# Optimization experiments

Measured on AMD Instinct MI355X. Metric: run time of the kernel, lower is better.

## Reference

```python
import jax, jax.numpy as jnp
import numpy as np

N_HEAD = 16
HEAD_DIM = 64  # n_embd // n_head = 1024 // 16

def setup_inputs() -> dict:
    key = jax.random.key(0)
    k1, k2, k3 = jax.random.split(key, 3)
    B, T, C = 4, 2048, 1024
    x = jax.random.normal(k1, (B, T, C), dtype=jnp.float32)
    w_qkv = jax.random.normal(k2, (3 * C, C), dtype=jnp.float32) * (C ** -0.5)
    w_proj = jax.random.normal(k3, (C, C), dtype=jnp.float32) * (C ** -0.5)
    b_proj = jnp.zeros((C,), dtype=jnp.float32)
    return {"x": x, "w_qkv": w_qkv, "w_proj": w_proj, "b_proj": b_proj}

def reference(x, w_qkv, w_proj, b_proj):
    B, T, C = x.shape
    H, hd = N_HEAD, HEAD_DIM
    # fused QKV projection (no bias), torch Linear: x @ W^T
    qkv = jnp.einsum('btc,dc->btd', x, w_qkv)           # [B,T,3C]
    # module-specific reshape: per-head groups of 3*hd, then chunk into q,k,v
    qkv = qkv.reshape(B, T, H, 3 * hd)
    q, k, v = jnp.split(qkv, 3, axis=-1)                # each [B,T,H,hd]
    q = q.transpose(0, 2, 1, 3)                         # [B,H,T,hd]
    k = k.transpose(0, 2, 1, 3)
    v = v.transpose(0, 2, 1, 3)
    att = jnp.einsum('bhqd,bhkd->bhqk', q, k) * (hd ** -0.5)
    causal = jnp.tril(jnp.ones((T, T), dtype=bool))
    att = jnp.where(causal, att, -jnp.inf)
    att = jax.nn.softmax(att, axis=-1)
    out = jnp.einsum('bhqk,bhkd->bhqd', att, v)         # [B,H,T,hd]
    out = out.transpose(0, 2, 1, 3).reshape(B, T, C)
    out = jnp.einsum('btc,dc->btd', out, w_proj) + b_proj
    return out
```

## Files before the change

### kernel.cpp

```cpp
#include <hip/hip_runtime.h>
#include <hip/hip_bf16.h>

typedef __attribute__((ext_vector_type(8))) short bf16x8;
typedef __attribute__((ext_vector_type(4))) float f32x4;
typedef __attribute__((ext_vector_type(16))) float f32x16;
typedef __attribute__((ext_vector_type(4))) int i32x4;
typedef unsigned short u16;

__device__ __forceinline__ u16 f2bf(float f) {
    __hip_bfloat16 h = __float2bfloat16(f);
    return __builtin_bit_cast(u16, h);
}
__device__ __forceinline__ bf16x8 load8(const u16* p) {
    return *reinterpret_cast<const bf16x8*>(p);
}
__device__ __forceinline__ void gl2lds16(const u16* g, u16* l) {
    __builtin_amdgcn_global_load_lds(
        (const __attribute__((address_space(1))) void*)g,
        (__attribute__((address_space(3))) void*)l, 16, 0, 0);
}
__device__ __forceinline__ unsigned int cvtpk(float lo, float hi) {
    unsigned int r;
    asm("v_cvt_pk_bf16_f32 %0, %1, %2" : "=v"(r) : "v"(lo), "v"(hi));
    return r;
}

#define QSCALE 0.1803368801111244f

__global__ __launch_bounds__(256) void cast_f32_bf16(
    const float* __restrict__ src, u16* __restrict__ dst, int n4)
{
    int i = blockIdx.x * blockDim.x + threadIdx.x;
    if (i < n4) {
        float4 f = reinterpret_cast<const float4*>(src)[i];
        ushort4 o;
        o.x = f2bf(f.x); o.y = f2bf(f.y); o.z = f2bf(f.z); o.w = f2bf(f.w);
        reinterpret_cast<ushort4*>(dst)[i] = o;
    }
}

#define GEMM128_BODY(EPILOGUE)                                                 \
    __shared__ __align__(16) u16 As[128 * 32];                                 \
    __shared__ __align__(16) u16 Bs[128 * 32];                                 \
    const int t = threadIdx.x;                                                 \
    const int lane = t & 63;                                                   \
    const int wave = t >> 6;                                                   \
    const int quad = lane >> 4;                                                \
    const int lid  = lane & 15;                                                \
    const int wrow = wave & 1;                                                 \
    const int wcol = wave >> 1;                                                \
    const int mtile = blockIdx.x * 128;                                        \
    const int ntile = blockIdx.y * 128;                                        \
    const int srow = t >> 2;                                                   \
    const int scol = (t & 3) * 8;                                              \
    const u16* ga0 = Aptr + (size_t)(mtile + srow) * 1024 + scol;              \
    const u16* ga1 = Aptr + (size_t)(mtile + 64 + srow) * 1024 + scol;         \
    const u16* gb0 = Bptr + (size_t)(ntile + srow) * 1024 + scol;              \
    const u16* gb1 = Bptr + (size_t)(ntile + 64 + srow) * 1024 + scol;         \
    u16* la0 = As + t * 8;                                                     \
    u16* la1 = As + (256 + t) * 8;                                             \
    u16* lb0 = Bs + t * 8;                                                     \
    u16* lb1 = Bs + (256 + t) * 8;                                             \
    f32x4 acc[4][4] = {};                                                      \
    const int aro = wrow * 64 * 32 + quad * 8;                                 \
    const int bro = wcol * 64 * 32 + quad * 8;                                 \
    for (int k0 = 0; k0 < 1024; k0 += 32) {                                    \
        __syncthreads();                                                       \
        gl2lds16(ga0 + k0, la0);                                               \
        gl2lds16(ga1 + k0, la1);                                               \
        gl2lds16(gb0 + k0, lb0);                                               \
        gl2lds16(gb1 + k0, lb1);                                               \
        __syncthreads();                                                       \
        bf16x8 a[4], b[4];                                                     \
        _Pragma("unroll")                                                      \
        for (int i = 0; i < 4; ++i) {                                          \
            a[i] = load8(As + aro + (i * 16 + lid) * 32);                      \
            b[i] = load8(Bs + bro + (i * 16 + lid) * 32);                      \
        }                                                                      \
        _Pragma("unroll")                                                      \
        for (int mi = 0; mi < 4; ++mi)                                         \
            _Pragma("unroll")                                                  \
            for (int ni = 0; ni < 4; ++ni)                                     \
                acc[mi][ni] = __builtin_amdgcn_mfma_f32_16x16x32_bf16(         \
                    a[mi], b[ni], acc[mi][ni], 0, 0, 0);                       \
    }                                                                          \
    EPILOGUE

__global__ __launch_bounds__(256) void qkv_gemm128(
    const u16* __restrict__ Aptr, const u16* __restrict__ Bptr,
    u16* __restrict__ Q, u16* __restrict__ K, u16* __restrict__ Vt)
{
    GEMM128_BODY(
    _Pragma("unroll")
    for (int mi = 0; mi < 4; ++mi)
        _Pragma("unroll")
        for (int ni = 0; ni < 4; ++ni)
            _Pragma("unroll")
            for (int r = 0; r < 4; ++r) {
                int m = mtile + wrow * 64 + mi * 16 + quad * 4 + r;
                int n = ntile + wcol * 64 + ni * 16 + lid;
                int h = n / 192;
                int rr = n - h * 192;
                int sel = rr >> 6;
                int d = rr & 63;
                float v = acc[mi][ni][r];
                if (sel == 2)
                    Vt[((size_t)h * 64 + d) * 8192 + m] = f2bf(v);
                else if (sel == 0)
                    Q[((size_t)h * 8192 + m) * 64 + d] = f2bf(v * QSCALE);
                else
                    K[((size_t)h * 8192 + m) * 64 + d] = f2bf(v);
            }
    )
}

__global__ __launch_bounds__(256) void proj_gemm128(
    const u16* __restrict__ Aptr, const u16* __restrict__ Bptr,
    const float* __restrict__ bias, float* __restrict__ out)
{
    GEMM128_BODY(
    _Pragma("unroll")
    for (int mi = 0; mi < 4; ++mi)
        _Pragma("unroll")
        for (int ni = 0; ni < 4; ++ni)
            _Pragma("unroll")
            for (int r = 0; r < 4; ++r) {
                int m = mtile + wrow * 64 + mi * 16 + quad * 4 + r;
                int n = ntile + wcol * 64 + ni * 16 + lid;
                out[(size_t)m * 1024 + n] = acc[mi][ni][r] + bias[n];
            }
    )
}

__global__ __launch_bounds__(256, 4) void attn(
    const u16* __restrict__ Q, const u16* __restrict__ K,
    const u16* __restrict__ Vtg, u16* __restrict__ O)
{
    const int qtile = 15 - (blockIdx.x >> 6);
    const int bh = blockIdx.x & 63;
    const int b = bh >> 4, h = bh & 15;
    const int tid = threadIdx.x;
    const int lane = tid & 63;
    const int wave = tid >> 6;
    const int c31 = lane & 31;
    const int ht  = lane >> 5;

    const size_t hb = ((size_t)h * 8192 + (size_t)b * 2048) * 64;
    const u16* Qp = Q + hb;
    const u16* Kp = K + hb;
    const u16* Vp = Vtg + (size_t)h * 64 * 8192 + (size_t)b * 2048;

    __shared__ __align__(16) u16 Vt[2][64 * 64];

    const int vd = tid >> 3, vslot = tid & 7;
    const int vchunk = vslot ^ (vd & 7);
    const u16* vg0 = Vp + (size_t)vd * 8192 + vchunk * 8;
    const u16* vg1 = vg0 + (size_t)32 * 8192;

    const int qb = qtile * 128;
    const int qw = qb + wave * 32;
    const int q  = qw + c31;

    bf16x8 qf[4];
#pragma unroll
    for (int dm = 0; dm < 4; ++dm)
        qf[dm] = load8(Qp + (size_t)q * 64 + dm * 16 + ht * 8);

    f32x16 od0 = {}, od1 = {};
    float lsum = 0.f;

    const int nkt   = 2 * qtile + 2;
    const int nkt_w = 2 * qtile + ((wave < 2) ? 1 : 2);

    gl2lds16(vg0, Vt[0] + tid * 8);
    gl2lds16(vg1, Vt[0] + 2048 + tid * 8);

#define SOFTMAX_KB(ST, KBOFF, PF0, PF1)                                        \
    {                                                                          \
        float pv[16];                                                          \
        _Pragma("unroll")                                                      \
        for (int r = 0; r < 16; ++r) {                                         \
            const int kg = k0 + (KBOFF) + (r & 3) + 8 * (r >> 2) + 4 * ht;     \
            float sv = ST[r];                                                  \
            if (needmask && kg > q) sv = -1e30f;                               \
            const float p = exp2f(sv);                                         \
            pv[r] = p;                                                         \
            lsum += p;                                                         \
        }                                                                      \
        _Pragma("unroll")                                                      \
        for (int a = 0; a < 2; ++a) {                                          \
            unsigned int u  = cvtpk(pv[8 * a + 0], pv[8 * a + 1]);             \
            unsigned int u2 = cvtpk(pv[8 * a + 2], pv[8 * a + 3]);             \
            unsigned int v  = cvtpk(pv[8 * a + 4], pv[8 * a + 5]);             \
            unsigned int v2 = cvtpk(pv[8 * a + 6], pv[8 * a + 7]);             \
            int r1 = __shfl_xor((int)(ht ? u : v), 32, 64);                    \
            int r2 = __shfl_xor((int)(ht ? u2 : v2), 32, 64);                  \
            i32x4 w;                                                           \
            w.x = ht ? r1 : (int)u;                                            \
            w.y = ht ? r2 : (int)u2;                                           \
            w.z = ht ? (int)v : r1;                                            \
            w.w = ht ? (int)v2 : r2;                                           \
            ((a) ? (PF1) : (PF0)) = __builtin_bit_cast(bf16x8, w);             \
        }                                                                      \
    }

    for (int kt = 0; kt < nkt; ++kt) {
        const int k0 = kt * 64;
        u16* vbuf = Vt[kt & 1];
        const bool active = kt < nkt_w;
        bf16x8 pf[4];

        if (active) {
            const bool needmask = (k0 + 63 > qw);
            bf16x8 kfA[4], kfB[4];
#pragma unroll
            for (int dm = 0; dm < 4; ++dm)
                kfA[dm] = load8(Kp + (size_t)(k0 + c31) * 64 + dm * 16 + ht * 8);
#pragma unroll
            for (int dm = 0; dm < 4; ++dm)
                kfB[dm] = load8(Kp + (size_t)(k0 + 32 + c31) * 64 + dm * 16 + ht * 8);

            f32x16 stA = {}, stB = {};
            __builtin_amdgcn_s_setprio(1);
#pragma unroll
            for (int dm = 0; dm < 4; ++dm)
                stA = __builtin_amdgcn_mfma_f32_32x32x16_bf16(kfA[dm], qf[dm], stA, 0, 0, 0);
#pragma unroll
            for (int dm = 0; dm < 4; ++dm)
                stB = __builtin_amdgcn_mfma_f32_32x32x16_bf16(kfB[dm], qf[dm], stB, 0, 0, 0);
            __builtin_amdgcn_s_setprio(0);

            SOFTMAX_KB(stA, 0,  pf[0], pf[1]);
            SOFTMAX_KB(stB, 32, pf[2], pf[3]);
        }

        __syncthreads();

        if (kt + 1 < nkt) {
            const int kn = k0 + 64;
            u16* vnext = Vt[(kt + 1) & 1];
            gl2lds16(vg0 + kn, vnext + tid * 8);
            gl2lds16(vg1 + kn, vnext + 2048 + tid * 8);
        }

        if (active) {
            __builtin_amdgcn_s_setprio(1);
#pragma unroll
            for (int km = 0; km < 4; ++km) {
                const int sl = ((km * 2 + ht) ^ (c31 & 7)) * 8;
                bf16x8 v0 = load8(vbuf + c31 * 64 + sl);
                bf16x8 v1 = load8(vbuf + (32 + c31) * 64 + sl);
                od0 = __builtin_amdgcn_mfma_f32_32x32x16_bf16(v0, pf[km], od0, 0, 0, 0);
                od1 = __builtin_amdgcn_mfma_f32_32x32x16_bf16(v1, pf[km], od1, 0, 0, 0);
            }
            __builtin_amdgcn_s_setprio(0);
        }
    }

    const float tot = lsum +
        __builtin_bit_cast(float, __shfl_xor(__builtin_bit_cast(int, lsum), 32, 64));
    const float inv = 1.0f / tot;

    const size_t orow = (size_t)(b * 2048 + q) * 1024 + h * 64;
#pragma unroll
    for (int tp = 0; tp < 8; ++tp) {
        const int r = 2 * tp;
        const int d = (r & 3) + 8 * (r >> 2) + 4 * ht;
        unsigned int w0 = (unsigned int)f2bf(od0[r] * inv) |
                          ((unsigned int)f2bf(od0[r + 1] * inv) << 16);
        unsigned int w1 = (unsigned int)f2bf(od1[r] * inv) |
                          ((unsigned int)f2bf(od1[r + 1] * inv) << 16);
        *reinterpret_cast<unsigned int*>(const_cast<u16*>(O) + orow + d) = w0;
        *reinterpret_cast<unsigned int*>(const_cast<u16*>(O) + orow + 32 + d) = w1;
    }
#undef SOFTMAX_KB
}

extern "C" void kernel_launch(void* const* d_in, const int* in_sizes, int n_in,
                              void* d_out, int out_size, void* d_ws, size_t ws_size,
                              hipStream_t stream) {
    const float* x      = (const float*)d_in[0];
    const float* w_qkv  = (const float*)d_in[1];
    const float* w_proj = (const float*)d_in[2];
    const float* b_proj = (const float*)d_in[3];
    float* out = (float*)d_out;

    u16* Q   = (u16*)d_ws;
    u16* K   = Q   + (size_t)16 * 8192 * 64;
    u16* Vt  = K   + (size_t)16 * 8192 * 64;
    u16* A2  = Vt  + (size_t)16 * 64 * 8192;
    u16* Xb  = A2  + (size_t)8192 * 1024;
    u16* Wqb = Xb  + (size_t)8192 * 1024;
    u16* Wpb = Wqb + (size_t)3072 * 1024;

    cast_f32_bf16<<<dim3(8192), 256, 0, stream>>>(x, Xb, 8192 * 1024 / 4);
    cast_f32_bf16<<<dim3(3072), 256, 0, stream>>>(w_qkv, Wqb, 3072 * 1024 / 4);
    cast_f32_bf16<<<dim3(1024), 256, 0, stream>>>(w_proj, Wpb, 1024 * 1024 / 4);

    qkv_gemm128<<<dim3(64, 24), 256, 0, stream>>>(Xb, Wqb, Q, K, Vt);
    attn<<<dim3(1024), 256, 0, stream>>>(Q, K, Vt, A2);
    proj_gemm128<<<dim3(64, 8), 256, 0, stream>>>(A2, Wpb, b_proj, out);
}
```

Measured before the change: 295.9 us.

## Shrink attention blocks to 64 queries with two waves and skip masked half-tiles

The attention kernel now runs 2048 blocks of 128 threads, each covering a 64-row query tile with two waves instead of a 128-row tile with four. Each thread stages four V chunks into LDS instead of two. The per-wave inactive-iteration logic is replaced by skipping the second 32-key half of a tile, both the QK MFMA and the PV MFMA, when it lies entirely above the diagonal. This is meant to cut causal waste and improve load balance across CUs, at the cost of more blocks, more K/V reloads per query, and fewer waves to hide latency per block.

```diff
diff --git a/kernel.cpp b/kernel.cpp
--- a/kernel.cpp
+++ b/kernel.cpp
@@ -132,11 +132,11 @@
     )
 }
 
-__global__ __launch_bounds__(256, 4) void attn(
+__global__ __launch_bounds__(128, 4) void attn(
     const u16* __restrict__ Q, const u16* __restrict__ K,
     const u16* __restrict__ Vtg, u16* __restrict__ O)
 {
-    const int qtile = 15 - (blockIdx.x >> 6);
+    const int qt64 = 31 - (blockIdx.x >> 6);
     const int bh = blockIdx.x & 63;
     const int b = bh >> 4, h = bh & 15;
     const int tid = threadIdx.x;
@@ -154,11 +154,18 @@
 
     const int vd = tid >> 3, vslot = tid & 7;
     const int vchunk = vslot ^ (vd & 7);
-    const u16* vg0 = Vp + (size_t)vd * 8192 + vchunk * 8;
-    const u16* vg1 = vg0 + (size_t)32 * 8192;
-
-    const int qb = qtile * 128;
-    const int qw = qb + wave * 32;
+    const u16* vg = Vp + (size_t)vd * 8192 + vchunk * 8;
+    u16* const ldst = (u16*)Vt[0] + vd * 64 + vslot * 8;
+
+#define STAGE(BUFSEL, KK)                                                      \
+    {                                                                          \
+        u16* d_ = ldst + (BUFSEL) * 4096;                                      \
+        _Pragma("unroll")                                                      \
+        for (int g = 0; g < 4; ++g)                                            \
+            gl2lds16(vg + (size_t)g * 16 * 8192 + (KK), d_ + g * 1024);        \
+    }
+
+    const int qw = qt64 * 64 + wave * 32;
     const int q  = qw + c31;
 
     bf16x8 qf[4];
@@ -169,11 +176,9 @@
     f32x16 od0 = {}, od1 = {};
     float lsum = 0.f;
 
-    const int nkt   = 2 * qtile + 2;
-    const int nkt_w = 2 * qtile + ((wave < 2) ? 1 : 2);
-
-    gl2lds16(vg0, Vt[0] + tid * 8);
-    gl2lds16(vg1, Vt[0] + 2048 + tid * 8);
+    const int nkt = qt64 + 1;
+
+    STAGE(0, 0)
 
 #define SOFTMAX_KB(ST, KBOFF, PF0, PF1)                                        \
     {                                                                          \
@@ -207,54 +212,52 @@
     for (int kt = 0; kt < nkt; ++kt) {
         const int k0 = kt * 64;
         u16* vbuf = Vt[kt & 1];
-        const bool active = kt < nkt_w;
+        const bool skipB = (k0 >= qw);
+        const bool needmask = (k0 + 63 > qw);
         bf16x8 pf[4];
 
-        if (active) {
-            const bool needmask = (k0 + 63 > qw);
-            bf16x8 kfA[4], kfB[4];
+        {
+            bf16x8 kfA[4];
 #pragma unroll
             for (int dm = 0; dm < 4; ++dm)
                 kfA[dm] = load8(Kp + (size_t)(k0 + c31) * 64 + dm * 16 + ht * 8);
+            f32x16 stA = {};
+            __builtin_amdgcn_s_setprio(1);
+#pragma unroll
+            for (int dm = 0; dm < 4; ++dm)
+                stA = __builtin_amdgcn_mfma_f32_32x32x16_bf16(kfA[dm], qf[dm], stA, 0, 0, 0);
+            __builtin_amdgcn_s_setprio(0);
+            SOFTMAX_KB(stA, 0, pf[0], pf[1]);
+        }
+        if (!skipB) {
+            bf16x8 kfB[4];
 #pragma unroll
             for (int dm = 0; dm < 4; ++dm)
                 kfB[dm] = load8(Kp + (size_t)(k0 + 32 + c31) * 64 + dm * 16 + ht * 8);
-
-            f32x16 stA = {}, stB = {};
+            f32x16 stB = {};
             __builtin_amdgcn_s_setprio(1);
-#pragma unroll
-            for (int dm = 0; dm < 4; ++dm)
-                stA = __builtin_amdgcn_mfma_f32_32x32x16_bf16(kfA[dm], qf[dm], stA, 0, 0, 0);
 #pragma unroll
             for (int dm = 0; dm < 4; ++dm)
                 stB = __builtin_amdgcn_mfma_f32_32x32x16_bf16(kfB[dm], qf[dm], stB, 0, 0, 0);
             __builtin_amdgcn_s_setprio(0);
-
-            SOFTMAX_KB(stA, 0,  pf[0], pf[1]);
             SOFTMAX_KB(stB, 32, pf[2], pf[3]);
         }
 
         __syncthreads();
 
-        if (kt + 1 < nkt) {
-            const int kn = k0 + 64;
-            u16* vnext = Vt[(kt + 1) & 1];
-            gl2lds16(vg0 + kn, vnext + tid * 8);
-            gl2lds16(vg1 + kn, vnext + 2048 + tid * 8);
+        if (kt + 1 < nkt) STAGE((kt + 1) & 1, k0 + 64)
+
+        __builtin_amdgcn_s_setprio(1);
+#pragma unroll
+        for (int km = 0; km < 4; ++km) {
+            if (km >= 2 && skipB) continue;
+            const int sl = ((km * 2 + ht) ^ (c31 & 7)) * 8;
+            bf16x8 v0 = load8(vbuf + c31 * 64 + sl);
+            bf16x8 v1 = load8(vbuf + (32 + c31) * 64 + sl);
+            od0 = __builtin_amdgcn_mfma_f32_32x32x16_bf16(v0, pf[km], od0, 0, 0, 0);
+            od1 = __builtin_amdgcn_mfma_f32_32x32x16_bf16(v1, pf[km], od1, 0, 0, 0);
         }
-
-        if (active) {
-            __builtin_amdgcn_s_setprio(1);
-#pragma unroll
-            for (int km = 0; km < 4; ++km) {
-                const int sl = ((km * 2 + ht) ^ (c31 & 7)) * 8;
-                bf16x8 v0 = load8(vbuf + c31 * 64 + sl);
-                bf16x8 v1 = load8(vbuf + (32 + c31) * 64 + sl);
-                od0 = __builtin_amdgcn_mfma_f32_32x32x16_bf16(v0, pf[km], od0, 0, 0, 0);
-                od1 = __builtin_amdgcn_mfma_f32_32x32x16_bf16(v1, pf[km], od1, 0, 0, 0);
-            }
-            __builtin_amdgcn_s_setprio(0);
-        }
+        __builtin_amdgcn_s_setprio(0);
     }
 
     const float tot = lsum +
@@ -274,6 +277,7 @@
         *reinterpret_cast<unsigned int*>(const_cast<u16*>(O) + orow + 32 + d) = w1;
     }
 #undef SOFTMAX_KB
+#undef STAGE
 }
 
 extern "C" void kernel_launch(void* const* d_in, const int* in_sizes, int n_in,
@@ -298,6 +302,6 @@
     cast_f32_bf16<<<dim3(1024), 256, 0, stream>>>(w_proj, Wpb, 1024 * 1024 / 4);
 
     qkv_gemm128<<<dim3(64, 24), 256, 0, stream>>>(Xb, Wqb, Q, K, Vt);
-    attn<<<dim3(1024), 256, 0, stream>>>(Q, K, Vt, A2);
+    attn<<<dim3(2048), 128, 0, stream>>>(Q, K, Vt, A2);
     proj_gemm128<<<dim3(64, 8), 256, 0, stream>>>(A2, Wpb, b_proj, out);
 }
```

Result: faster. 289.2 us (-2.3%).
